# Kernel tuning notes

Hardware: AMD Instinct MI355X
Metric: run time of the kernel (lower is better)

The kernel has to match this reference:

```python
import jax, jax.numpy as jnp
import numpy as np

B, L, D = 4, 2048, 1024
DI = D            # d_inner = expand * d_model, expand=1
N = 8             # d_state
K = 4             # d_conv
R = 64            # dt_rank = ceil(d_model/16)
EPS = 1e-5


def setup_inputs() -> dict:
    key = jax.random.key(0)
    ks = jax.random.split(key, 10)
    hidden_states = jax.random.normal(ks[0], (B, L, D), dtype=jnp.float32)
    norm_w = jnp.ones((D,), dtype=jnp.float32)
    in_proj_w = jax.random.normal(ks[1], (2 * DI, D), dtype=jnp.float32) * 0.02
    conv_w = jax.random.normal(ks[2], (DI, 1, K), dtype=jnp.float32) * 0.2
    conv_b = jnp.zeros((DI,), dtype=jnp.float32)
    x_proj_w = jax.random.normal(ks[3], (R + 2 * N, DI), dtype=jnp.float32) * 0.02
    dt_proj_w = jax.random.normal(ks[4], (DI, R), dtype=jnp.float32) * 0.1
    # bias init so softplus(bias) lands in a sane dt range (~e^-4 .. e^-1)
    dt_proj_b = jax.random.uniform(ks[5], (DI,), minval=-4.0, maxval=-1.0, dtype=jnp.float32)
    # S4D-real style init: A = -[1..N] per channel
    A_log = jnp.log(jnp.broadcast_to(jnp.arange(1, N + 1, dtype=jnp.float32), (DI, N)))
    D_skip = jnp.ones((DI,), dtype=jnp.float32)
    out_proj_w = jax.random.normal(ks[6], (D, DI), dtype=jnp.float32) * 0.02
    return {
        "hidden_states": hidden_states, "norm_w": norm_w,
        "in_proj_w": in_proj_w, "conv_w": conv_w, "conv_b": conv_b,
        "x_proj_w": x_proj_w, "dt_proj_w": dt_proj_w, "dt_proj_b": dt_proj_b,
        "A_log": A_log, "D_skip": D_skip, "out_proj_w": out_proj_w,
    }


def _rmsnorm(x, w):
    return x * jax.lax.rsqrt(jnp.mean(x * x, axis=-1, keepdims=True) + EPS) * w


def _mamba_block(hidden_states, norm_w, in_proj_w, conv_w, conv_b,
                 x_proj_w, dt_proj_w, dt_proj_b, A_log, D_skip, out_proj_w):
    x = _rmsnorm(hidden_states, norm_w)                      # [B,L,D]
    xz = jnp.einsum('bld,ed->ble', x, in_proj_w)             # [B,L,2*DI]
    x, z = jnp.split(xz, 2, axis=-1)                         # [B,L,DI] each
    # causal depthwise conv1d (torch pads d_conv-1 both sides then slices :L => left pad only)
    xc = jnp.transpose(x, (0, 2, 1))                         # [B,DI,L]
    k = conv_w.shape[-1]
    xc = jax.lax.conv_general_dilated(
        xc, conv_w, window_strides=(1,), padding=[(k - 1, 0)],
        dimension_numbers=('NCH', 'OIH', 'NCH'), feature_group_count=DI)
    x = jax.nn.silu(jnp.transpose(xc, (0, 2, 1)) + conv_b)   # [B,L,DI]
    # input-dependent dt, B, C
    dbl = jnp.einsum('bld,ed->ble', x, x_proj_w)             # [B,L,R+2N]
    dt, Bm, Cm = jnp.split(dbl, [R, R + N], axis=-1)
    dt = jax.nn.softplus(jnp.einsum('blr,dr->bld', dt, dt_proj_w) + dt_proj_b)  # [B,L,DI]
    A = -jnp.exp(A_log)                                      # [DI,N]
    dA = jnp.exp(dt[..., None] * A)                          # [B,L,DI,N]
    dBx = dt[..., None] * Bm[:, :, None, :] * x[..., None]   # [B,L,DI,N]

    def step(h, inp):
        a_t, bx_t, c_t = inp                                 # [B,DI,N],[B,DI,N],[B,N]
        h = a_t * h + bx_t
        y = jnp.einsum('bdn,bn->bd', h, c_t)
        return h, y

    h0 = jnp.zeros((hidden_states.shape[0], DI, N), dtype=x.dtype)
    _, ys = jax.lax.scan(step, h0, (jnp.transpose(dA, (1, 0, 2, 3)),
                                    jnp.transpose(dBx, (1, 0, 2, 3)),
                                    jnp.transpose(Cm, (1, 0, 2))))
    y = jnp.transpose(ys, (1, 0, 2)) + D_skip * x            # [B,L,DI]
    y = y * jax.nn.silu(z)
    out = jnp.einsum('bld,ed->ble', y, out_proj_w)           # [B,L,D]
    return out  # use_res=False


def reference(hidden_states, norm_w, in_proj_w, conv_w, conv_b,
              x_proj_w, dt_proj_w, dt_proj_b, A_log, D_skip, out_proj_w):
    return _mamba_block(hidden_states, norm_w, in_proj_w, conv_w, conv_b,
                        x_proj_w, dt_proj_w, dt_proj_b, A_log, D_skip, out_proj_w)
```

## Files before the change

kernel.cpp:

```cpp
#include <hip/hip_runtime.h>
#include <stdint.h>
#include <stddef.h>


typedef unsigned short u16;
typedef unsigned int u32;
typedef _Float16 f16;
typedef __attribute__((ext_vector_type(8))) _Float16 half8;
typedef __attribute__((ext_vector_type(4))) _Float16 half4;
typedef __attribute__((ext_vector_type(4))) float f32x4;

#define LSEQ 2048
#define DMODEL 1024
#define NSTATE 8
#define NCHUNK 32
#define CHUNKL 64
#define NROWS 8192
#define WS_NEED (99ull << 20)

__device__ __forceinline__ void gload_lds16(const void* g, void* l) {
    __builtin_amdgcn_global_load_lds((__attribute__((address_space(1))) void*)g,
                                     (__attribute__((address_space(3))) void*)l,
                                     16, 0, 0);
}

__global__ __launch_bounds__(256) void sentinel_kernel(float* __restrict__ out, int n) {
    int i = blockIdx.x * 256 + threadIdx.x;
    if (i < n) out[i] = 999.0f;
}

#define T0 524288
#define T1 20480
#define T2 16384
#define T3 262144
#define WCVT_BLK 3216
#define ZERO_BLK 640
__global__ __launch_bounds__(256) void prep_kernel(const float* __restrict__ s0,
                                                   const float* __restrict__ s1,
                                                   const float* __restrict__ s2,
                                                   const float* __restrict__ s3,
                                                   f16* __restrict__ d0, f16* __restrict__ d1,
                                                   f16* __restrict__ d2, f16* __restrict__ d3,
                                                   float* __restrict__ dblz,
                                                   const float* __restrict__ X,
                                                   const float* __restrict__ W,
                                                   f16* __restrict__ O) {
    const int bx = blockIdx.x;
    const int tid = threadIdx.x;
    if (bx < WCVT_BLK) {
        int idx = bx * 256 + tid;
        const float* s; f16* d; int i;
        if (idx < T0) { s = s0; d = d0; i = idx; }
        else if (idx < T0 + T1) { s = s1; d = d1; i = idx - T0; }
        else if (idx < T0 + T1 + T2) { s = s2; d = d2; i = idx - T0 - T1; }
        else { s = s3; d = d3; i = idx - T0 - T1 - T2; }
        f32x4 v = *(const f32x4*)(s + (size_t)i * 4);
        half4 o; o[0] = (f16)v[0]; o[1] = (f16)v[1]; o[2] = (f16)v[2]; o[3] = (f16)v[3];
        *(half4*)(d + (size_t)i * 4) = o;
    } else if (bx < WCVT_BLK + ZERO_BLK) {
        int i = (bx - WCVT_BLK) * 256 + tid;
        const f32x4 z4 = {0.f, 0.f, 0.f, 0.f};
        ((f32x4*)dblz)[i] = z4;
    } else {
        const int row = bx - (WCVT_BLK + ZERO_BLK);
        f32x4 u = *(const f32x4*)(X + (size_t)row * DMODEL + tid * 4);
        float ss = u[0]*u[0] + u[1]*u[1] + u[2]*u[2] + u[3]*u[3];
        for (int off = 32; off; off >>= 1) ss += __shfl_down(ss, off, 64);
        __shared__ float red[4];
        if ((tid & 63) == 0) red[tid >> 6] = ss;
        __syncthreads();
        float tot = red[0] + red[1] + red[2] + red[3];
        float scale = rsqrtf(tot * (1.0f / DMODEL) + 1e-5f);
        f32x4 w = *(const f32x4*)(W + tid * 4);
        half4 o;
        o[0] = (f16)(u[0] * scale * w[0]); o[1] = (f16)(u[1] * scale * w[1]);
        o[2] = (f16)(u[2] * scale * w[2]); o[3] = (f16)(u[3] * scale * w[3]);
        *(half4*)(O + (size_t)row * DMODEL + tid * 4) = o;
    }
}

template <int EPI, int AF32>
__global__ __launch_bounds__(256) void gemm_f16(const void* __restrict__ Ap, int lda,
                                                const f16* __restrict__ Bm, int ldb,
                                                void* __restrict__ C0, void* __restrict__ C1,
                                                int ldc, int N, int klen,
                                                const float* __restrict__ fbias) {
    __shared__ alignas(16) f16 sA[128 * 64];
    __shared__ alignas(16) f16 sB[128 * 64];
    const int tid = threadIdx.x;
    const int wave = tid >> 6, lane = tid & 63;
    const int wm = (wave >> 1) * 64, wn = (wave & 1) * 64;
    const int tm = blockIdx.x, tn = blockIdx.y;
    const int q = lane >> 4, cl = lane & 15;
    const int kbeg = blockIdx.z * klen;

    f32x4 acc[4][4];
    const f32x4 zero4 = {0.f, 0.f, 0.f, 0.f};
#pragma unroll
    for (int t = 0; t < 4; t++)
#pragma unroll
        for (int u = 0; u < 4; u++) acc[t][u] = zero4;

    int rS[4], gkS[4];
#pragma unroll
    for (int j = 0; j < 4; j++) {
        int c = wave * 256 + j * 64 + lane;
        rS[j] = c >> 3;
        gkS[j] = (c & 7) ^ (rS[j] & 7);
    }

    for (int k0 = kbeg; k0 < kbeg + klen; k0 += 64) {
        __syncthreads();
#pragma unroll
        for (int j = 0; j < 4; j++) {
            int ldsoff = (wave * 256 + j * 64) * 8;
            if (!AF32) {
                int ga = tm * 128 + rS[j];
                gload_lds16((const f16*)Ap + (size_t)ga * lda + k0 + gkS[j] * 8, sA + ldsoff);
            }
            int gb = tn * 128 + rS[j];
            if (gb >= N) gb = N - 1;
            gload_lds16(Bm + (size_t)gb * ldb + k0 + gkS[j] * 8, sB + ldsoff);
        }
        __syncthreads();

        half8 af[4][2], bf[4][2];
#pragma unroll
        for (int t = 0; t < 4; t++)
#pragma unroll
            for (int s = 0; s < 2; s++) {
                int m = wm + t * 16 + cl;
                int kc = s * 4 + q;
                if (AF32) {
                    const float* pa = (const float*)Ap + (size_t)(tm * 128 + m) * lda + k0 + kc * 8;
                    f32x4 v0 = *(const f32x4*)pa, v1 = *(const f32x4*)(pa + 4);
                    half8 a;
                    a[0] = (f16)v0[0]; a[1] = (f16)v0[1]; a[2] = (f16)v0[2]; a[3] = (f16)v0[3];
                    a[4] = (f16)v1[0]; a[5] = (f16)v1[1]; a[6] = (f16)v1[2]; a[7] = (f16)v1[3];
                    af[t][s] = a;
                } else {
                    af[t][s] = *(const half8*)(sA + m * 64 + ((kc ^ (m & 7)) << 3));
                }
                int n = wn + t * 16 + cl;
                bf[t][s] = *(const half8*)(sB + n * 64 + ((kc ^ (n & 7)) << 3));
            }
#pragma unroll
        for (int t = 0; t < 4; t++)
#pragma unroll
            for (int u = 0; u < 4; u++) {
                acc[t][u] = __builtin_amdgcn_mfma_f32_16x16x32_f16(af[t][0], bf[u][0], acc[t][u], 0, 0, 0);
                acc[t][u] = __builtin_amdgcn_mfma_f32_16x16x32_f16(af[t][1], bf[u][1], acc[t][u], 0, 0, 0);
            }
    }

    const int rowbase = tm * 128 + wm + q * 4;
    const int colbase = tn * 128 + wn + cl;
#pragma unroll
    for (int t = 0; t < 4; t++)
#pragma unroll
        for (int r = 0; r < 4; r++) {
            size_t rb_ = (size_t)(rowbase + t * 16 + r) * ldc;
            size_t rb1 = (size_t)(rowbase + t * 16 + r) * 1024;
#pragma unroll
            for (int u = 0; u < 4; u++) {
                int gcol = colbase + u * 16;
                float v = acc[t][u][r];
                if (EPI == 0) {
                    if (gcol < 1024) ((f16*)C0)[rb1 + gcol] = (f16)v;
                    else             ((f16*)C1)[rb1 + gcol - 1024] = (f16)v;
                } else if (EPI == 1) {
                    if (gcol < N) ((float*)C0)[rb_ + gcol] = v;
                } else if (EPI == 2) {
                    if (gcol < N) atomicAdd((float*)C0 + rb_ + gcol, v);
                } else {
                    if (gcol < N) {
                        float sv = v + fbias[gcol];
                        sv = (sv > 15.f) ? sv : log1pf(__expf(sv));
                        ((f16*)C0)[rb_ + gcol] = (f16)sv;
                    }
                }
            }
        }
}

__global__ __launch_bounds__(256) void conv_silu_kernel(const f16* __restrict__ x,
                                                        const float* __restrict__ cw,
                                                        const float* __restrict__ cb,
                                                        f16* __restrict__ xc) {
    const int rg = blockIdx.x;
    const int d = blockIdx.y * 256 + threadIdx.x;
    const int row0 = rg * 4;
    const int l0 = row0 & (LSEQ - 1);
    float w0 = cw[d * 4], w1 = cw[d * 4 + 1], w2 = cw[d * 4 + 2], w3 = cw[d * 4 + 3];
    float bias = cb[d];
    float v[7];
#pragma unroll
    for (int j = 0; j < 7; j++) {
        int ll = l0 - 3 + j;
        v[j] = (ll >= 0) ? (float)x[(size_t)(row0 - 3 + j) * 1024 + d] : 0.f;
    }
#pragma unroll
    for (int i = 0; i < 4; i++) {
        float acc = bias + w0 * v[i] + w1 * v[i + 1] + w2 * v[i + 2] + w3 * v[i + 3];
        xc[(size_t)(row0 + i) * 1024 + d] = (f16)(acc / (1.f + __expf(-acc)));
    }
}

__global__ __launch_bounds__(256) void scan1_kernel(const f16* __restrict__ dt,
                                                    const f16* __restrict__ xc,
                                                    const float* __restrict__ dbl,
                                                    const float* __restrict__ A_log,
                                                    float* __restrict__ hF,
                                                    float* __restrict__ Pb) {
    const int d = blockIdx.x * 256 + threadIdx.x;
    const int c = blockIdx.y;
    const int b = blockIdx.z;
    __shared__ float sB[CHUNKL * NSTATE];
    for (int i = threadIdx.x; i < CHUNKL * NSTATE; i += 256)
        sB[i] = dbl[(size_t)(b * LSEQ + c * CHUNKL + (i >> 3)) * 80 + 64 + (i & 7)];
    __syncthreads();
    float Aa[NSTATE];
#pragma unroll
    for (int n = 0; n < NSTATE; n++) Aa[n] = -__expf(A_log[d * NSTATE + n]);
    float h[NSTATE], P[NSTATE];
#pragma unroll
    for (int n = 0; n < NSTATE; n++) { h[n] = 0.f; P[n] = 1.f; }
    for (int li = 0; li < CHUNKL; li++) {
        size_t rowb = (size_t)(b * LSEQ + c * CHUNKL + li);
        float dtv = (float)dt[rowb * 1024 + d];
        float xv = (float)xc[rowb * 1024 + d];
        float dtx = dtv * xv;
#pragma unroll
        for (int n = 0; n < NSTATE; n++) {
            float e = __expf(Aa[n] * dtv);
            h[n] = e * h[n] + dtx * sB[li * 8 + n];
            P[n] *= e;
        }
    }
    size_t base = ((size_t)(b * 1024 + d) * NCHUNK + c) * NSTATE;
#pragma unroll
    for (int n = 0; n < NSTATE; n++) { hF[base + n] = h[n]; Pb[base + n] = P[n]; }
}

__global__ __launch_bounds__(256) void scan2_kernel(const f16* __restrict__ dt,
                                                    const f16* __restrict__ xc,
                                                    const float* __restrict__ dbl,
                                                    const float* __restrict__ A_log,
                                                    const float* __restrict__ hF,
                                                    const float* __restrict__ Pb,
                                                    const f16* __restrict__ z,
                                                    const float* __restrict__ Dsk,
                                                    f16* __restrict__ yout) {
    const int d = blockIdx.x * 256 + threadIdx.x;
    const int c = blockIdx.y;
    const int b = blockIdx.z;
    __shared__ float sB[CHUNKL * NSTATE];
    __shared__ float sC[CHUNKL * NSTATE];
    for (int i = threadIdx.x; i < CHUNKL * NSTATE; i += 256) {
        size_t rb = (size_t)(b * LSEQ + c * CHUNKL + (i >> 3)) * 80;
        sB[i] = dbl[rb + 64 + (i & 7)];
        sC[i] = dbl[rb + 72 + (i & 7)];
    }
    __syncthreads();
    float Aa[NSTATE];
#pragma unroll
    for (int n = 0; n < NSTATE; n++) Aa[n] = -__expf(A_log[d * NSTATE + n]);
    float h[NSTATE];
#pragma unroll
    for (int n = 0; n < NSTATE; n++) h[n] = 0.f;
    {
        size_t dbase = (size_t)(b * 1024 + d) * NCHUNK * NSTATE;
        for (int cc = 0; cc < c; cc++) {
            size_t base = dbase + (size_t)cc * NSTATE;
#pragma unroll
            for (int n = 0; n < NSTATE; n++)
                h[n] = Pb[base + n] * h[n] + hF[base + n];
        }
    }
    const float dval = Dsk[d];
    for (int li = 0; li < CHUNKL; li++) {
        size_t rowb = (size_t)(b * LSEQ + c * CHUNKL + li);
        float dtv = (float)dt[rowb * 1024 + d];
        float xv = (float)xc[rowb * 1024 + d];
        float dtx = dtv * xv;
        float y = 0.f;
#pragma unroll
        for (int n = 0; n < NSTATE; n++) {
            float e = __expf(Aa[n] * dtv);
            h[n] = e * h[n] + dtx * sB[li * 8 + n];
            y += h[n] * sC[li * 8 + n];
        }
        y += dval * xv;
        float zv = (float)z[rowb * 1024 + d];
        y *= zv / (1.f + __expf(-zv));
        yout[rowb * 1024 + d] = (f16)y;
    }
}

extern "C" void kernel_launch(void* const* d_in, const int* in_sizes, int n_in,
                              void* d_out, int out_size, void* d_ws, size_t ws_size,
                              hipStream_t stream) {
    (void)in_sizes; (void)n_in;
    const float* hidden    = (const float*)d_in[0];
    const float* norm_w    = (const float*)d_in[1];
    const float* in_proj_w = (const float*)d_in[2];
    const float* conv_w    = (const float*)d_in[3];
    const float* conv_b    = (const float*)d_in[4];
    const float* x_proj_w  = (const float*)d_in[5];
    const float* dt_proj_w = (const float*)d_in[6];
    const float* dt_proj_b = (const float*)d_in[7];
    const float* A_log     = (const float*)d_in[8];
    const float* D_skip    = (const float*)d_in[9];
    const float* out_proj_w= (const float*)d_in[10];
    float* out = (float*)d_out;

    if (ws_size < WS_NEED) {
        sentinel_kernel<<<dim3((out_size + 255) / 256), 256, 0, stream>>>(out, out_size);
        return;
    }

    char* ws = (char*)d_ws;
    f16*   xn_h  = (f16*)(ws);
    f16*   xbuf_h= (f16*)(ws + (16ull << 20));
    f16*   zbuf_h= (f16*)(ws + (32ull << 20));
    f16*   xc_h  = (f16*)(ws + (48ull << 20));
    f16*   wih   = (f16*)(ws + (64ull << 20));
    f16*   woh   = (f16*)(ws + (68ull << 20));
    f16*   wxh   = (f16*)(ws + (70ull << 20));
    f16*   wdh   = (f16*)(ws + (70ull << 20) + (512ull << 10));
    float* dbl_f = (float*)(ws + (71ull << 20));
    f16*   dth   = (f16*)(ws + (75ull << 20));
    float* hF    = (float*)(ws + (91ull << 20));
    float* Pb    = (float*)(ws + (95ull << 20));
    f16*   y_h   = xn_h;

    prep_kernel<<<dim3(WCVT_BLK + ZERO_BLK + NROWS), 256, 0, stream>>>(
        in_proj_w, x_proj_w, dt_proj_w, out_proj_w, wih, wxh, wdh, woh,
        dbl_f, hidden, norm_w, xn_h);
    gemm_f16<0, 0><<<dim3(64, 16), 256, 0, stream>>>(xn_h, 1024, wih, 1024,
                                                     xbuf_h, zbuf_h, 1024, 2048, 1024, nullptr);
    conv_silu_kernel<<<dim3(NROWS / 4, 4), 256, 0, stream>>>(xbuf_h, conv_w, conv_b, xc_h);
    gemm_f16<2, 0><<<dim3(64, 1, 4), 256, 0, stream>>>(xc_h, 1024, wxh, 1024,
                                                       dbl_f, nullptr, 80, 80, 256, nullptr);
    gemm_f16<3, 1><<<dim3(64, 8), 256, 0, stream>>>(dbl_f, 80, wdh, 64,
                                                    dth, nullptr, 1024, 1024, 64, dt_proj_b);
    scan1_kernel<<<dim3(4, NCHUNK, 4), 256, 0, stream>>>(dth, xc_h, dbl_f, A_log, hF, Pb);
    scan2_kernel<<<dim3(4, NCHUNK, 4), 256, 0, stream>>>(dth, xc_h, dbl_f, A_log, hF, Pb,
                                                         zbuf_h, D_skip, y_h);
    gemm_f16<1, 0><<<dim3(64, 8), 256, 0, stream>>>(y_h, 1024, woh, 1024,
                                                    out, nullptr, 1024, 1024, 1024, nullptr);
}
```

Baseline: 332.1 us.

## Add separate chunk-state combine kernel, halve scan chunk length, batch loads

Halves the chunk length so the two scan passes launch twice as many blocks. A new combine kernel computes each chunk's initial state once, so every scan2 block no longer replays the prefix of earlier chunk states on its own. The chunk-state layout becomes chunk-major with vectorized stores and loads, and the dt/x/z loads are batched eight timesteps at a time to expose memory-level parallelism. The cost is an extra kernel launch, a sequential 64-step combine pass, and more workspace.

```diff
diff --git a/kernel.cpp b/kernel.cpp
--- a/kernel.cpp
+++ b/kernel.cpp
@@ -13,10 +13,10 @@
 #define LSEQ 2048
 #define DMODEL 1024
 #define NSTATE 8
-#define NCHUNK 32
-#define CHUNKL 64
+#define NCHUNK 64
+#define CHUNKL 32
 #define NROWS 8192
-#define WS_NEED (99ull << 20)
+#define WS_NEED (115ull << 20)
 
 __device__ __forceinline__ void gload_lds16(const void* g, void* l) {
     __builtin_amdgcn_global_load_lds((__attribute__((address_space(1))) void*)g,
@@ -216,38 +216,64 @@
     const int c = blockIdx.y;
     const int b = blockIdx.z;
     __shared__ float sB[CHUNKL * NSTATE];
-    for (int i = threadIdx.x; i < CHUNKL * NSTATE; i += 256)
-        sB[i] = dbl[(size_t)(b * LSEQ + c * CHUNKL + (i >> 3)) * 80 + 64 + (i & 7)];
+    sB[threadIdx.x] = dbl[(size_t)(b * LSEQ + c * CHUNKL + (threadIdx.x >> 3)) * 80 + 64 + (threadIdx.x & 7)];
     __syncthreads();
+    f32x4 al0 = *(const f32x4*)(A_log + d * 8);
+    f32x4 al1 = *(const f32x4*)(A_log + d * 8 + 4);
     float Aa[NSTATE];
 #pragma unroll
-    for (int n = 0; n < NSTATE; n++) Aa[n] = -__expf(A_log[d * NSTATE + n]);
+    for (int n = 0; n < 4; n++) { Aa[n] = -__expf(al0[n]); Aa[n + 4] = -__expf(al1[n]); }
     float h[NSTATE], P[NSTATE];
 #pragma unroll
     for (int n = 0; n < NSTATE; n++) { h[n] = 0.f; P[n] = 1.f; }
-    for (int li = 0; li < CHUNKL; li++) {
-        size_t rowb = (size_t)(b * LSEQ + c * CHUNKL + li);
-        float dtv = (float)dt[rowb * 1024 + d];
-        float xv = (float)xc[rowb * 1024 + d];
-        float dtx = dtv * xv;
-#pragma unroll
-        for (int n = 0; n < NSTATE; n++) {
-            float e = __expf(Aa[n] * dtv);
-            h[n] = e * h[n] + dtx * sB[li * 8 + n];
-            P[n] *= e;
-        }
-    }
-    size_t base = ((size_t)(b * 1024 + d) * NCHUNK + c) * NSTATE;
-#pragma unroll
-    for (int n = 0; n < NSTATE; n++) { hF[base + n] = h[n]; Pb[base + n] = P[n]; }
+    const f16* pdt = dt + (size_t)(b * LSEQ + c * CHUNKL) * 1024 + d;
+    const f16* pxc = xc + (size_t)(b * LSEQ + c * CHUNKL) * 1024 + d;
+    for (int lb = 0; lb < CHUNKL; lb += 8) {
+        float vdt[8], vxc[8];
+#pragma unroll
+        for (int j = 0; j < 8; j++) {
+            vdt[j] = (float)pdt[(size_t)(lb + j) * 1024];
+            vxc[j] = (float)pxc[(size_t)(lb + j) * 1024];
+        }
+#pragma unroll
+        for (int j = 0; j < 8; j++) {
+            float dtx = vdt[j] * vxc[j];
+#pragma unroll
+            for (int n = 0; n < NSTATE; n++) {
+                float e = __expf(Aa[n] * vdt[j]);
+                h[n] = e * h[n] + dtx * sB[(lb + j) * 8 + n];
+                P[n] *= e;
+            }
+        }
+    }
+    size_t base = ((size_t)(c * 4 + b) * 1024 + d) * 8;
+    f32x4 o;
+    o[0]=h[0]; o[1]=h[1]; o[2]=h[2]; o[3]=h[3]; *(f32x4*)(hF + base) = o;
+    o[0]=h[4]; o[1]=h[5]; o[2]=h[6]; o[3]=h[7]; *(f32x4*)(hF + base + 4) = o;
+    o[0]=P[0]; o[1]=P[1]; o[2]=P[2]; o[3]=P[3]; *(f32x4*)(Pb + base) = o;
+    o[0]=P[4]; o[1]=P[5]; o[2]=P[6]; o[3]=P[7]; *(f32x4*)(Pb + base + 4) = o;
+}
+
+__global__ __launch_bounds__(256) void combine_kernel(const float* __restrict__ hF,
+                                                      const float* __restrict__ Pb,
+                                                      float* __restrict__ h0) {
+    int t = blockIdx.x * 256 + threadIdx.x;
+    int n = t & 7, dd = (t >> 3) & 1023, b = t >> 13;
+    size_t off = (size_t)(b * 1024 + dd) * 8 + n;
+    float h = 0.f;
+#pragma unroll 8
+    for (int c = 0; c < NCHUNK; c++) {
+        size_t idx = (size_t)c * 32768 + off;
+        h0[idx] = h;
+        h = fmaf(Pb[idx], h, hF[idx]);
+    }
 }
 
 __global__ __launch_bounds__(256) void scan2_kernel(const f16* __restrict__ dt,
                                                     const f16* __restrict__ xc,
                                                     const float* __restrict__ dbl,
                                                     const float* __restrict__ A_log,
-                                                    const float* __restrict__ hF,
-                                                    const float* __restrict__ Pb,
+                                                    const float* __restrict__ h0,
                                                     const f16* __restrict__ z,
                                                     const float* __restrict__ Dsk,
                                                     f16* __restrict__ yout) {
@@ -256,44 +282,53 @@
     const int b = blockIdx.z;
     __shared__ float sB[CHUNKL * NSTATE];
     __shared__ float sC[CHUNKL * NSTATE];
-    for (int i = threadIdx.x; i < CHUNKL * NSTATE; i += 256) {
-        size_t rb = (size_t)(b * LSEQ + c * CHUNKL + (i >> 3)) * 80;
-        sB[i] = dbl[rb + 64 + (i & 7)];
-        sC[i] = dbl[rb + 72 + (i & 7)];
+    {
+        size_t rb = (size_t)(b * LSEQ + c * CHUNKL + (threadIdx.x >> 3)) * 80;
+        sB[threadIdx.x] = dbl[rb + 64 + (threadIdx.x & 7)];
+        sC[threadIdx.x] = dbl[rb + 72 + (threadIdx.x & 7)];
     }
     __syncthreads();
+    f32x4 al0 = *(const f32x4*)(A_log + d * 8);
+    f32x4 al1 = *(const f32x4*)(A_log + d * 8 + 4);
     float Aa[NSTATE];
 #pragma unroll
-    for (int n = 0; n < NSTATE; n++) Aa[n] = -__expf(A_log[d * NSTATE + n]);
+    for (int n = 0; n < 4; n++) { Aa[n] = -__expf(al0[n]); Aa[n + 4] = -__expf(al1[n]); }
     float h[NSTATE];
-#pragma unroll
-    for (int n = 0; n < NSTATE; n++) h[n] = 0.f;
     {
-        size_t dbase = (size_t)(b * 1024 + d) * NCHUNK * NSTATE;
-        for (int cc = 0; cc < c; cc++) {
-            size_t base = dbase + (size_t)cc * NSTATE;
-#pragma unroll
-            for (int n = 0; n < NSTATE; n++)
-                h[n] = Pb[base + n] * h[n] + hF[base + n];
-        }
+        size_t base = ((size_t)(c * 4 + b) * 1024 + d) * 8;
+        f32x4 h0a = *(const f32x4*)(h0 + base);
+        f32x4 h0b = *(const f32x4*)(h0 + base + 4);
+#pragma unroll
+        for (int n = 0; n < 4; n++) { h[n] = h0a[n]; h[n + 4] = h0b[n]; }
     }
     const float dval = Dsk[d];
-    for (int li = 0; li < CHUNKL; li++) {
-        size_t rowb = (size_t)(b * LSEQ + c * CHUNKL + li);
-        float dtv = (float)dt[rowb * 1024 + d];
-        float xv = (float)xc[rowb * 1024 + d];
-        float dtx = dtv * xv;
-        float y = 0.f;
-#pragma unroll
-        for (int n = 0; n < NSTATE; n++) {
-            float e = __expf(Aa[n] * dtv);
-            h[n] = e * h[n] + dtx * sB[li * 8 + n];
-            y += h[n] * sC[li * 8 + n];
-        }
-        y += dval * xv;
-        float zv = (float)z[rowb * 1024 + d];
-        y *= zv / (1.f + __expf(-zv));
-        yout[rowb * 1024 + d] = (f16)y;
+    const size_t rowoff = (size_t)(b * LSEQ + c * CHUNKL) * 1024 + d;
+    const f16* pdt = dt + rowoff;
+    const f16* pxc = xc + rowoff;
+    const f16* pz  = z  + rowoff;
+    f16* py = yout + rowoff;
+    for (int lb = 0; lb < CHUNKL; lb += 8) {
+        float vdt[8], vxc[8], vz[8];
+#pragma unroll
+        for (int j = 0; j < 8; j++) {
+            vdt[j] = (float)pdt[(size_t)(lb + j) * 1024];
+            vxc[j] = (float)pxc[(size_t)(lb + j) * 1024];
+            vz[j]  = (float)pz[(size_t)(lb + j) * 1024];
+        }
+#pragma unroll
+        for (int j = 0; j < 8; j++) {
+            float dtx = vdt[j] * vxc[j];
+            float y = 0.f;
+#pragma unroll
+            for (int n = 0; n < NSTATE; n++) {
+                float e = __expf(Aa[n] * vdt[j]);
+                h[n] = e * h[n] + dtx * sB[(lb + j) * 8 + n];
+                y += h[n] * sC[(lb + j) * 8 + n];
+            }
+            y += dval * vxc[j];
+            y *= vz[j] / (1.f + __expf(-vz[j]));
+            py[(size_t)(lb + j) * 1024] = (f16)y;
+        }
     }
 }
 
@@ -331,7 +366,8 @@
     float* dbl_f = (float*)(ws + (71ull << 20));
     f16*   dth   = (f16*)(ws + (75ull << 20));
     float* hF    = (float*)(ws + (91ull << 20));
-    float* Pb    = (float*)(ws + (95ull << 20));
+    float* Pb    = (float*)(ws + (99ull << 20));
+    float* h0    = (float*)(ws + (107ull << 20));
     f16*   y_h   = xn_h;
 
     prep_kernel<<<dim3(WCVT_BLK + ZERO_BLK + NROWS), 256, 0, stream>>>(
@@ -345,7 +381,8 @@
     gemm_f16<3, 1><<<dim3(64, 8), 256, 0, stream>>>(dbl_f, 80, wdh, 64,
                                                     dth, nullptr, 1024, 1024, 64, dt_proj_b);
     scan1_kernel<<<dim3(4, NCHUNK, 4), 256, 0, stream>>>(dth, xc_h, dbl_f, A_log, hF, Pb);
-    scan2_kernel<<<dim3(4, NCHUNK, 4), 256, 0, stream>>>(dth, xc_h, dbl_f, A_log, hF, Pb,
+    combine_kernel<<<dim3(128), 256, 0, stream>>>(hF, Pb, h0);
+    scan2_kernel<<<dim3(4, NCHUNK, 4), 256, 0, stream>>>(dth, xc_h, dbl_f, A_log, h0,
                                                          zbuf_h, D_skip, y_h);
     gemm_f16<1, 0><<<dim3(64, 8), 256, 0, stream>>>(y_h, 1024, woh, 1024,
                                                     out, nullptr, 1024, 1024, 1024, nullptr);
```

Result: faster. 295.8 us (-10.9%).
